# Kernel optimization log

Measured on AMD Instinct MI355X. Metric: run time of the kernel, lower is better.

The kernel has to match this reference:

```python
import jax, jax.numpy as jnp
import numpy as np
from jax import lax

E, D, I, K = 8, 1024, 2048, 2
B, S = 4, 1024


def setup_inputs() -> dict:
    key = jax.random.key(0)
    k1, k2, k3, k4, k5 = jax.random.split(key, 5)
    x = jax.random.normal(k1, (B, S, D), dtype=jnp.float32)
    routing_weights = jax.random.uniform(k2, (B, S, K), dtype=jnp.float32)
    selected_experts = jax.random.randint(k3, (B, S, K), 0, E).astype(jnp.int64)
    w1 = 0.02 * jax.random.normal(k4, (E, D, I), dtype=jnp.float32)
    w2 = 0.02 * jax.random.normal(k5, (E, I, D), dtype=jnp.float32)
    return {"x": x, "routing_weights": routing_weights,
            "selected_experts": selected_experts, "w1": w1, "w2": w2}


def reference(x, routing_weights, selected_experts, w1, w2):
    shape = x.shape
    d = shape[-1]
    xf = x.reshape(-1, d)                       # [T, D]
    rw = routing_weights.reshape(xf.shape[0], -1)   # [T, K]
    se = selected_experts.reshape(xf.shape[0], -1)  # [T, K]
    n_experts = w1.shape[0]

    def body(acc, inputs):
        e, w1e, w2e = inputs
        # per-token combine weight for expert e (rw assumed >= 0; zero weight == not routed)
        wt = jnp.sum(jnp.where(se == e, rw, 0.0), axis=-1)  # [T]
        h = jax.nn.silu(xf @ w1e)                # [T, I]
        out = h @ w2e                            # [T, D]
        return acc + out * wt[:, None], None

    acc0 = jnp.zeros_like(xf)
    acc, _ = lax.scan(body, acc0, (jnp.arange(n_experts), w1, w2))
    return acc.reshape(shape)
```

## Files before the change

### kernel.cpp

```cpp
#include <hip/hip_runtime.h>
#include <stdint.h>

#define E_EXPERTS 8
#define D_DIM 1024
#define I_DIM 2048
#define T_TOKENS 4096
#define NSLOTS 8192
#define TILE 128
#define MAXPAD (NSLOTS + E_EXPERTS * TILE)
#define TPX 9

#define XCVT_BLOCKS 2048
#define WT_BLOCKS 2048
#define PREP_GRID (1 + XCVT_BLOCKS + 2 * WT_BLOCKS)

typedef __attribute__((ext_vector_type(8))) short bf16x8;
typedef __attribute__((ext_vector_type(4))) float f32x4;

__device__ __forceinline__ unsigned short f2b(float f) {
  union { float f; uint32_t u; } v; v.f = f;
  uint32_t r = v.u + 0x7FFFu + ((v.u >> 16) & 1u);
  return (unsigned short)(r >> 16);
}
__device__ __forceinline__ float b2f(unsigned short u) {
  union { uint32_t u; float f; } v; v.u = ((uint32_t)u) << 16; return v.f;
}

__device__ __forceinline__ void async16(const unsigned short* g, unsigned short* l) {
  __builtin_amdgcn_global_load_lds(
      (const __attribute__((address_space(1))) void*)g,
      (__attribute__((address_space(3))) void*)l, 16, 0, 0);
}

__global__ __launch_bounds__(256) void prep_k(
    const float* __restrict__ x, const float* __restrict__ w1, const float* __restrict__ w2,
    const int* __restrict__ se,
    unsigned short* __restrict__ xb, unsigned short* __restrict__ w1t,
    unsigned short* __restrict__ w2t,
    int* __restrict__ ntiles, int* __restrict__ desc,
    int* __restrict__ tok, int* __restrict__ slot_of) {
  int b = blockIdx.x;
  int tid = threadIdx.x;

  if (b == 0) {
    __shared__ int scnt[E_EXPERTS], sbase[E_EXPERTS + 1], scur[E_EXPERTS];
    if (tid < E_EXPERTS) scnt[tid] = 0;
    __syncthreads();
    for (int s = tid; s < NSLOTS; s += 256) atomicAdd(&scnt[se[s]], 1);
    __syncthreads();
    if (tid == 0) {
      int acc = 0, nt = 0;
      for (int e = 0; e < E_EXPERTS; e++) {
        int n = scnt[e];
        sbase[e] = acc;
        scur[e] = acc;
        int pad = (n + TILE - 1) & ~(TILE - 1);
        for (int m = 0; m * TILE < pad; m++) { desc[2 * nt] = e; desc[2 * nt + 1] = acc + m * TILE; nt++; }
        acc += pad;
      }
      sbase[E_EXPERTS] = acc;
      *ntiles = nt;
    }
    __syncthreads();
    for (int e = 0; e < E_EXPERTS; e++) {
      int s0 = sbase[e] + scnt[e], s1 = sbase[e + 1];
      for (int s = s0 + tid; s < s1; s += 256) tok[s] = 0;
    }
    for (int s = tid; s < NSLOTS; s += 256) {
      int e = se[s];
      int pos = atomicAdd(&scur[e], 1);
      tok[pos] = s >> 1;
      slot_of[s] = pos;
    }
    return;
  }

  int bb = b - 1;
  int sec = bb >> 11;
  int sub = bb & 2047;

  if (sec == 0) {
    size_t i = ((size_t)sub * 256 + tid) * 8;
    float4 v0 = *(const float4*)(x + i);
    float4 v1 = *(const float4*)(x + i + 4);
    ushort4 o0, o1;
    o0.x = f2b(v0.x); o0.y = f2b(v0.y); o0.z = f2b(v0.z); o0.w = f2b(v0.w);
    o1.x = f2b(v1.x); o1.y = f2b(v1.y); o1.z = f2b(v1.z); o1.w = f2b(v1.w);
    *(ushort4*)(xb + i) = o0;
    *(ushort4*)(xb + i + 4) = o1;
    return;
  }

  const float* src; unsigned short* dst; int R, C;
  if (sec == 1) { src = w1; dst = w1t; R = D_DIM; C = I_DIM; }
  else          { src = w2; dst = w2t; R = I_DIM; C = D_DIM; }
  int e = sub >> 8, t = sub & 255;
  int ctiles = C / 128;
  int r0b = (t / ctiles) * 64, c0b = (t % ctiles) * 128;

  int lane = tid & 63, wave = tid >> 6;
  int c0 = c0b + wave * 32 + (lane >> 4) * 8;
  int r0 = r0b + (lane & 15) * 4;

  size_t eoff = (size_t)e * R * C;
  const float* s0 = src + eoff + (size_t)r0 * C + c0;

  float4 v[4][2];
#pragma unroll
  for (int i = 0; i < 4; i++) {
    v[i][0] = *(const float4*)(s0 + (size_t)i * C);
    v[i][1] = *(const float4*)(s0 + (size_t)i * C + 4);
  }

  unsigned short* d0 = dst + eoff + (size_t)c0 * R + r0;
#pragma unroll
  for (int j = 0; j < 8; j++) {
    ushort4 o;
    o.x = f2b(((const float*)&v[0][j >> 2])[j & 3]);
    o.y = f2b(((const float*)&v[1][j >> 2])[j & 3]);
    o.z = f2b(((const float*)&v[2][j >> 2])[j & 3]);
    o.w = f2b(((const float*)&v[3][j >> 2])[j & 3]);
    *(ushort4*)(d0 + (size_t)j * R) = o;
  }
}

template <int KLEN, int ASTR, int BSTR, int NDIM, int PHASE>
__global__ __launch_bounds__(256) void moe_gemm_k(
    const unsigned short* __restrict__ Amat, const unsigned short* __restrict__ Bt,
    const int* __restrict__ desc, const int* __restrict__ ntiles_p,
    const int* __restrict__ tok, unsigned short* __restrict__ Hout) {
  int id = blockIdx.x;
  int xcd = id & 7, r = id >> 3;
  int ti = xcd * TPX + r % TPX;
  int q = r / TPX;
  int nb, kh;
  if (PHASE == 1) { nb = q; kh = 0; }
  else           { kh = q & 1; nb = q >> 1; }
  if (ti >= *ntiles_p) return;
  int e = desc[2 * ti];
  int slot0 = desc[2 * ti + 1];

  const unsigned short* Bbase = Bt + (size_t)e * NDIM * BSTR + (size_t)nb * 128 * BSTR + kh * KLEN;

  __shared__ unsigned short As[128 * 64];
  __shared__ unsigned short Bs[128 * 64];

  int tid = threadIdx.x;
  int lane = tid & 63;
  int wave = tid >> 6;
  int wm = (wave >> 1) * 64, wn = (wave & 1) * 64;
  int l15 = lane & 15, quad = lane >> 4;

  f32x4 acc[4][4] = {};

  int sr = tid >> 3;
  int ldoff = (((lane & 7) ^ (lane >> 3)) * 8);

  const unsigned short* arow[4];
  const unsigned short* brow[4];
#pragma unroll
  for (int p = 0; p < 4; p++) {
    int rr = sr + p * 32;
    int row = (PHASE == 1) ? tok[slot0 + rr] : (slot0 + rr);
    arow[p] = Amat + (size_t)row * ASTR + kh * KLEN + ldoff;
    brow[p] = Bbase + (size_t)rr * BSTR + ldoff;
  }

  for (int kt = 0; kt < KLEN / 64; kt++) {
    int k0 = kt * 64;
#pragma unroll
    for (int p = 0; p < 4; p++) {
      unsigned short* adst = As + (size_t)(p * 256 + wave * 64) * 8;
      unsigned short* bdst = Bs + (size_t)(p * 256 + wave * 64) * 8;
      async16(arow[p] + k0, adst);
      async16(brow[p] + k0, bdst);
    }
    __syncthreads();
#pragma unroll
    for (int ks = 0; ks < 2; ks++) {
      bf16x8 af[4], bfr[4];
#pragma unroll
      for (int i = 0; i < 4; i++) {
        int rr = wm + i * 16 + l15;
        int cc = (((ks * 4 + quad) ^ (rr & 7)) * 8);
        af[i] = *(const bf16x8*)&As[rr * 64 + cc];
      }
#pragma unroll
      for (int j = 0; j < 4; j++) {
        int rr = wn + j * 16 + l15;
        int cc = (((ks * 4 + quad) ^ (rr & 7)) * 8);
        bfr[j] = *(const bf16x8*)&Bs[rr * 64 + cc];
      }
#pragma unroll
      for (int i = 0; i < 4; i++)
#pragma unroll
        for (int j = 0; j < 4; j++)
          acc[i][j] = __builtin_amdgcn_mfma_f32_16x16x32_bf16(af[i], bfr[j], acc[i][j], 0, 0, 0);
    }
    __syncthreads();
  }

#pragma unroll
  for (int i = 0; i < 4; i++) {
    int slotr = slot0 + wm + i * 16 + quad * 4;
#pragma unroll
    for (int rg = 0; rg < 4; rg++) {
      int row = slotr + rg;
      size_t base = (PHASE == 1) ? (size_t)row * NDIM
                                 : ((size_t)kh * MAXPAD + row) * NDIM;
#pragma unroll
      for (int j = 0; j < 4; j++) {
        int col = nb * 128 + wn + j * 16 + l15;
        float v = acc[i][j][rg];
        if (PHASE == 1) v = v / (1.f + __expf(-v));
        Hout[base + col] = f2b(v);
      }
    }
  }
}

__global__ void combine_k(const unsigned short* __restrict__ y, const float* __restrict__ rw,
                          const int* __restrict__ slot_of, float* __restrict__ out) {
  int g = blockIdx.x * blockDim.x + threadIdx.x;
  int t = g >> 7, dd = (g & 127) * 8;
  int s0 = slot_of[2 * t], s1 = slot_of[2 * t + 1];
  float w0 = rw[2 * t], w1 = rw[2 * t + 1];
  const unsigned short* p00 = y + (size_t)s0 * D_DIM + dd;
  const unsigned short* p01 = y + ((size_t)MAXPAD + s0) * D_DIM + dd;
  const unsigned short* p10 = y + (size_t)s1 * D_DIM + dd;
  const unsigned short* p11 = y + ((size_t)MAXPAD + s1) * D_DIM + dd;
  ushort4 a0 = *(const ushort4*)p00, a1 = *(const ushort4*)(p00 + 4);
  ushort4 b0 = *(const ushort4*)p01, b1 = *(const ushort4*)(p01 + 4);
  ushort4 c0 = *(const ushort4*)p10, c1 = *(const ushort4*)(p10 + 4);
  ushort4 d0 = *(const ushort4*)p11, d1 = *(const ushort4*)(p11 + 4);
  float4 o0, o1;
  o0.x = w0 * (b2f(a0.x) + b2f(b0.x)) + w1 * (b2f(c0.x) + b2f(d0.x));
  o0.y = w0 * (b2f(a0.y) + b2f(b0.y)) + w1 * (b2f(c0.y) + b2f(d0.y));
  o0.z = w0 * (b2f(a0.z) + b2f(b0.z)) + w1 * (b2f(c0.z) + b2f(d0.z));
  o0.w = w0 * (b2f(a0.w) + b2f(b0.w)) + w1 * (b2f(c0.w) + b2f(d0.w));
  o1.x = w0 * (b2f(a1.x) + b2f(b1.x)) + w1 * (b2f(c1.x) + b2f(d1.x));
  o1.y = w0 * (b2f(a1.y) + b2f(b1.y)) + w1 * (b2f(c1.y) + b2f(d1.y));
  o1.z = w0 * (b2f(a1.z) + b2f(b1.z)) + w1 * (b2f(c1.z) + b2f(d1.z));
  o1.w = w0 * (b2f(a1.w) + b2f(b1.w)) + w1 * (b2f(c1.w) + b2f(d1.w));
  float* op = out + (size_t)t * D_DIM + dd;
  *(float4*)op = o0;
  *(float4*)(op + 4) = o1;
}

extern "C" void kernel_launch(void* const* d_in, const int* in_sizes, int n_in,
                              void* d_out, int out_size, void* d_ws, size_t ws_size,
                              hipStream_t stream) {
  (void)in_sizes; (void)n_in; (void)ws_size; (void)out_size;
  const float* x  = (const float*)d_in[0];
  const float* rw = (const float*)d_in[1];
  const int*   se = (const int*)d_in[2];
  const float* w1 = (const float*)d_in[3];
  const float* w2 = (const float*)d_in[4];
  float* out = (float*)d_out;
  char* ws = (char*)d_ws;

  int* ntiles  = (int*)(ws + 128);
  int* desc    = (int*)(ws + 256);
  int* tok     = (int*)(ws + 4096);
  int* slot_of = (int*)(ws + 40960);
  unsigned short* xb   = (unsigned short*)(ws + 131072);
  unsigned short* w1t  = xb + (size_t)T_TOKENS * D_DIM;
  unsigned short* w2t  = w1t + (size_t)E_EXPERTS * D_DIM * I_DIM;
  unsigned short* hbuf = w2t + (size_t)E_EXPERTS * D_DIM * I_DIM;
  unsigned short* ypart = xb;

  prep_k<<<PREP_GRID, 256, 0, stream>>>(x, w1, w2, se, xb, w1t, w2t,
                                        ntiles, desc, tok, slot_of);
  moe_gemm_k<1024, 1024, 1024, I_DIM, 1><<<8 * TPX * (I_DIM / 128), 256, 0, stream>>>(
      xb, w1t, desc, ntiles, tok, hbuf);
  moe_gemm_k<1024, 2048, 2048, D_DIM, 2><<<8 * TPX * (D_DIM / 128) * 2, 256, 0, stream>>>(
      hbuf, w2t, desc, ntiles, tok, ypart);

  combine_k<<<T_TOKENS * 128 / 256, 256, 0, stream>>>(ypart, rw, slot_of, out);
}
```

Measured before the change: 295.9 us.

## Pre-pack transposed weights into swizzled 128x64 tiles for contiguous GEMM loads

The prep kernel now transposes each weight tile through an LDS buffer and writes it out as a contiguous 8192-element block. The bf16 layout inside each block already carries the XOR swizzle the GEMM expects. The GEMM then fetches B with fully contiguous per-thread 16-byte async loads instead of strided row loads, cutting address math and scattered accesses. The cost is an extra LDS round trip in the prep transpose, where the ts[(c*8+t)*129+rr] reads may hit bank conflicts.

```diff
diff --git a/kernel.cpp b/kernel.cpp
--- a/kernel.cpp
+++ b/kernel.cpp
@@ -11,8 +11,7 @@
 #define TPX 9
 
 #define XCVT_BLOCKS 2048
-#define WT_BLOCKS 2048
-#define PREP_GRID (1 + XCVT_BLOCKS + 2 * WT_BLOCKS)
+#define PREP_GRID (1 + XCVT_BLOCKS + 4096)
 
 typedef __attribute__((ext_vector_type(8))) short bf16x8;
 typedef __attribute__((ext_vector_type(4))) float f32x4;
@@ -76,11 +75,9 @@
   }
 
   int bb = b - 1;
-  int sec = bb >> 11;
-  int sub = bb & 2047;
-
-  if (sec == 0) {
-    size_t i = ((size_t)sub * 256 + tid) * 8;
+
+  if (bb < XCVT_BLOCKS) {
+    size_t i = ((size_t)bb * 256 + tid) * 8;
     float4 v0 = *(const float4*)(x + i);
     float4 v1 = *(const float4*)(x + i + 4);
     ushort4 o0, o1;
@@ -91,40 +88,47 @@
     return;
   }
 
-  const float* src; unsigned short* dst; int R, C;
-  if (sec == 1) { src = w1; dst = w1t; R = D_DIM; C = I_DIM; }
-  else          { src = w2; dst = w2t; R = I_DIM; C = D_DIM; }
-  int e = sub >> 8, t = sub & 255;
-  int ctiles = C / 128;
-  int r0b = (t / ctiles) * 64, c0b = (t % ctiles) * 128;
-
-  int lane = tid & 63, wave = tid >> 6;
-  int c0 = c0b + wave * 32 + (lane >> 4) * 8;
-  int r0 = r0b + (lane & 15) * 4;
-
-  size_t eoff = (size_t)e * R * C;
-  const float* s0 = src + eoff + (size_t)r0 * C + c0;
-
-  float4 v[4][2];
-#pragma unroll
-  for (int i = 0; i < 4; i++) {
-    v[i][0] = *(const float4*)(s0 + (size_t)i * C);
-    v[i][1] = *(const float4*)(s0 + (size_t)i * C + 4);
-  }
-
-  unsigned short* d0 = dst + eoff + (size_t)c0 * R + r0;
-#pragma unroll
-  for (int j = 0; j < 8; j++) {
-    ushort4 o;
-    o.x = f2b(((const float*)&v[0][j >> 2])[j & 3]);
-    o.y = f2b(((const float*)&v[1][j >> 2])[j & 3]);
-    o.z = f2b(((const float*)&v[2][j >> 2])[j & 3]);
-    o.w = f2b(((const float*)&v[3][j >> 2])[j & 3]);
-    *(ushort4*)(d0 + (size_t)j * R) = o;
-  }
-}
-
-template <int KLEN, int ASTR, int BSTR, int NDIM, int PHASE>
+  __shared__ float ts[64 * 129];
+  int wb = bb - XCVT_BLOCKS;
+  int mat = wb >> 11;
+  int sub = wb & 2047;
+  int e = sub >> 8, rem = sub & 255;
+  const float* src; unsigned short* dst; int C, k0, n0;
+  if (mat == 0) {
+    int nt = rem >> 4, kt = rem & 15;
+    C = I_DIM; k0 = kt * 64; n0 = nt * 128;
+    src = w1 + (size_t)e * D_DIM * I_DIM;
+    dst = w1t + ((size_t)((e * 16 + nt) * 16 + kt)) * 8192;
+  } else {
+    int nt = rem >> 5, kt = rem & 31;
+    C = D_DIM; k0 = kt * 64; n0 = nt * 128;
+    src = w2 + (size_t)e * D_DIM * I_DIM;
+    dst = w2t + ((size_t)((e * 8 + nt) * 32 + kt)) * 8192;
+  }
+
+#pragma unroll
+  for (int i = 0; i < 8; i++) {
+    int f4 = i * 256 + tid;
+    int row = f4 >> 5, c4 = (f4 & 31) * 4;
+    float4 v = *(const float4*)(src + (size_t)(k0 + row) * C + n0 + c4);
+    float* d = ts + row * 129 + c4;
+    d[0] = v.x; d[1] = v.y; d[2] = v.z; d[3] = v.w;
+  }
+  __syncthreads();
+#pragma unroll
+  for (int j = 0; j < 4; j++) {
+    int q = j * 256 + tid;
+    int rr = q >> 3, cc8 = q & 7;
+    int c = cc8 ^ (rr & 7);
+    bf16x8 o;
+#pragma unroll
+    for (int t = 0; t < 8; t++)
+      o[t] = (short)f2b(ts[(c * 8 + t) * 129 + rr]);
+    *(bf16x8*)(dst + (size_t)q * 8) = o;
+  }
+}
+
+template <int KLEN, int KFULL, int NDIM, int PHASE>
 __global__ __launch_bounds__(256) void moe_gemm_k(
     const unsigned short* __restrict__ Amat, const unsigned short* __restrict__ Bt,
     const int* __restrict__ desc, const int* __restrict__ ntiles_p,
@@ -140,8 +144,6 @@
   int e = desc[2 * ti];
   int slot0 = desc[2 * ti + 1];
 
-  const unsigned short* Bbase = Bt + (size_t)e * NDIM * BSTR + (size_t)nb * 128 * BSTR + kh * KLEN;
-
   __shared__ unsigned short As[128 * 64];
   __shared__ unsigned short Bs[128 * 64];
 
@@ -157,14 +159,15 @@
   int ldoff = (((lane & 7) ^ (lane >> 3)) * 8);
 
   const unsigned short* arow[4];
-  const unsigned short* brow[4];
 #pragma unroll
   for (int p = 0; p < 4; p++) {
     int rr = sr + p * 32;
     int row = (PHASE == 1) ? tok[slot0 + rr] : (slot0 + rr);
-    arow[p] = Amat + (size_t)row * ASTR + kh * KLEN + ldoff;
-    brow[p] = Bbase + (size_t)rr * BSTR + ldoff;
-  }
+    arow[p] = Amat + (size_t)row * KFULL + kh * KLEN + ldoff;
+  }
+  const unsigned short* Bpack =
+      Bt + ((((size_t)e * (NDIM / 128) + nb) * (KFULL / 64) + (size_t)kh * (KLEN / 64)) << 13) +
+      (size_t)tid * 8;
 
   for (int kt = 0; kt < KLEN / 64; kt++) {
     int k0 = kt * 64;
@@ -173,7 +176,7 @@
       unsigned short* adst = As + (size_t)(p * 256 + wave * 64) * 8;
       unsigned short* bdst = Bs + (size_t)(p * 256 + wave * 64) * 8;
       async16(arow[p] + k0, adst);
-      async16(brow[p] + k0, bdst);
+      async16(Bpack + (size_t)kt * 8192 + p * 2048, bdst);
     }
     __syncthreads();
 #pragma unroll
@@ -271,9 +274,9 @@
 
   prep_k<<<PREP_GRID, 256, 0, stream>>>(x, w1, w2, se, xb, w1t, w2t,
                                         ntiles, desc, tok, slot_of);
-  moe_gemm_k<1024, 1024, 1024, I_DIM, 1><<<8 * TPX * (I_DIM / 128), 256, 0, stream>>>(
+  moe_gemm_k<1024, 1024, I_DIM, 1><<<8 * TPX * (I_DIM / 128), 256, 0, stream>>>(
       xb, w1t, desc, ntiles, tok, hbuf);
-  moe_gemm_k<1024, 2048, 2048, D_DIM, 2><<<8 * TPX * (D_DIM / 128) * 2, 256, 0, stream>>>(
+  moe_gemm_k<1024, 2048, D_DIM, 2><<<8 * TPX * (D_DIM / 128) * 2, 256, 0, stream>>>(
       hbuf, w2t, desc, ntiles, tok, ypart);
 
   combine_k<<<T_TOKENS * 128 / 256, 256, 0, stream>>>(ypart, rw, slot_of, out);
```

Measured after the change: 294.5 us. About the same (-0.5%).
